# Optimization experiments

Measured on AMD Instinct MI355X. Metric: run time of the kernel, lower is better.

Reference implementation:

```python
import jax, jax.numpy as jnp
import numpy as np

N = 50000
E = 500000
CH = 256
H1, C1 = 4, 64
H2, C2 = 8, 32
CONCAT = H1 * C1 + H2 * C2  # 512


def setup_inputs() -> dict:
    key = jax.random.key(0)
    ks = jax.random.split(key, 16)
    s = 0.05
    x = jax.random.normal(ks[0], (N, CH), dtype=jnp.float32)
    edge_index = jax.random.randint(ks[1], (2, E), 0, N, dtype=jnp.int64)
    return {
        "x": x,
        "edge_index": edge_index,
        "gamma": jnp.ones((CH,), jnp.float32),
        "beta": jnp.zeros((CH,), jnp.float32),
        "W1": jax.random.normal(ks[2], (CH, H1 * C1), jnp.float32) * s,
        "a_src1": jax.random.normal(ks[3], (H1, C1), jnp.float32) * s,
        "a_dst1": jax.random.normal(ks[4], (H1, C1), jnp.float32) * s,
        "b1": jnp.zeros((H1 * C1,), jnp.float32),
        "W2": jax.random.normal(ks[5], (CH, H2 * C2), jnp.float32) * s,
        "a_src2": jax.random.normal(ks[6], (H2, C2), jnp.float32) * s,
        "a_dst2": jax.random.normal(ks[7], (H2, C2), jnp.float32) * s,
        "b2": jnp.zeros((H2 * C2,), jnp.float32),
        "Wu": jax.random.normal(ks[8], (CONCAT, CH), jnp.float32) * s,
        "bu": jnp.zeros((CH,), jnp.float32),
    }


def _layer_norm(x, gamma, beta, eps=1e-5):
    mu = jnp.mean(x, axis=-1, keepdims=True)
    var = jnp.var(x, axis=-1, keepdims=True)
    return (x - mu) * jax.lax.rsqrt(var + eps) * gamma + beta


def _gat_conv(x, src, dst, W, a_src, a_dst, bias, heads, out_ch, n_nodes):
    # x: [N, CH] -> per-head projection h: [N, H, C]
    h = (x @ W).reshape(n_nodes, heads, out_ch)
    alpha_s = jnp.einsum('nhc,hc->nh', h, a_src)  # [N, H]
    alpha_d = jnp.einsum('nhc,hc->nh', h, a_dst)  # [N, H]
    e = jax.nn.leaky_relu(alpha_s[src] + alpha_d[dst], negative_slope=0.2)  # [E, H]
    # segment softmax over incoming edges of each dst node (self-loops guarantee nonempty segments)
    m = jax.ops.segment_max(e, dst, num_segments=n_nodes)
    ex = jnp.exp(e - m[dst])
    denom = jax.ops.segment_sum(ex, dst, num_segments=n_nodes)
    a = ex / (denom[dst] + 1e-16)  # [E, H]
    msg = h[src] * a[:, :, None]  # [E, H, C]
    out = jax.ops.segment_sum(msg, dst, num_segments=n_nodes)  # [N, H, C]
    return out.reshape(n_nodes, heads * out_ch) + bias


def reference(x, edge_index, gamma, beta, W1, a_src1, a_dst1, b1,
              W2, a_src2, a_dst2, b2, Wu, bu):
    n = x.shape[0]
    # add self-loops (PyG GATConv default)
    loop = jnp.arange(n, dtype=edge_index.dtype)
    src = jnp.concatenate([edge_index[0], loop])
    dst = jnp.concatenate([edge_index[1], loop])

    residual = x
    x_norm = _layer_norm(x, gamma, beta)
    out1 = _gat_conv(x_norm, src, dst, W1, a_src1, a_dst1, b1, H1, C1, n)
    out2 = _gat_conv(x_norm, src, dst, W2, a_src2, a_dst2, b2, H2, C2, n)
    x_cat = jax.nn.elu(jnp.concatenate([out1, out2], axis=-1))
    unified = x_cat @ Wu + bu
    return residual + unified
```

## Files before the change

### kernel.cpp

```cpp
#include <hip/hip_runtime.h>
#include <hip/hip_bf16.h>
#include <math.h>

constexpr int CH = 256;
constexpr int CC = 512;
constexpr int AP = 16;
constexpr int HS = 576;

typedef __bf16 bf16x8 __attribute__((ext_vector_type(8)));
typedef float  f32x4  __attribute__((ext_vector_type(4)));
typedef float  f32x2  __attribute__((ext_vector_type(2)));
typedef int    i32x4  __attribute__((ext_vector_type(4)));
typedef __attribute__((address_space(3))) void lds_void;
typedef __attribute__((address_space(1))) void glb_void;

__device__ inline unsigned short f2bf(float f) {
    union { float f; unsigned u; } v; v.f = f;
    unsigned r = v.u + 0x7FFFu + ((v.u >> 16) & 1u);
    return (unsigned short)(r >> 16);
}
__device__ __host__ inline int perm_s2l(int s) {
    return (s & ~31) + 16 * (s & 1) + ((s & 31) >> 1);
}

__global__ void fused_pre_kernel(const float* __restrict__ x, const float* __restrict__ gamma,
                                 const float* __restrict__ beta,
                                 const float* __restrict__ W1, const float* __restrict__ W2,
                                 const float* __restrict__ Wu,
                                 const float* __restrict__ as1, const float* __restrict__ ad1,
                                 const float* __restrict__ as2, const float* __restrict__ ad2,
                                 const float* __restrict__ b1, const float* __restrict__ b2,
                                 unsigned short* __restrict__ xnb,
                                 unsigned short* __restrict__ WT1, unsigned short* __restrict__ WTu,
                                 unsigned short* __restrict__ Pt, float* __restrict__ bperm,
                                 int* __restrict__ deg,
                                 int N, int LNB) {
    int b = blockIdx.x;
    int t = threadIdx.x;
    if (b < LNB) {
        int wid = b * 4 + (t >> 6);
        int lane = t & 63;
        if (wid >= N) return;
        const float4 v = *(const float4*)(x + (size_t)wid * CH + lane * 4);
        float s = v.x + v.y + v.z + v.w;
        float sq = v.x * v.x + v.y * v.y + v.z * v.z + v.w * v.w;
        #pragma unroll
        for (int o = 32; o; o >>= 1) { s += __shfl_xor(s, o); sq += __shfl_xor(sq, o); }
        float mu = s * (1.0f / CH);
        float var = sq * (1.0f / CH) - mu * mu;
        float rs = rsqrtf(var + 1e-5f);
        float4 g = *(const float4*)(gamma + lane * 4);
        float4 bb = *(const float4*)(beta + lane * 4);
        unsigned short o0 = f2bf((v.x - mu) * rs * g.x + bb.x);
        unsigned short o1 = f2bf((v.y - mu) * rs * g.y + bb.y);
        unsigned short o2 = f2bf((v.z - mu) * rs * g.z + bb.z);
        unsigned short o3 = f2bf((v.w - mu) * rs * g.w + bb.w);
        uint2 pk;
        pk.x = (unsigned)o0 | ((unsigned)o1 << 16);
        pk.y = (unsigned)o2 | ((unsigned)o3 << 16);
        *(uint2*)(xnb + (size_t)wid * CH + lane * 4) = pk;
    } else if (b < LNB + 512) {
        int idx = (b - LNB) * 256 + t;
        int n = idx >> 8, k = idx & 255;
        float v = (n < 256) ? W1[(size_t)k * 256 + n] : W2[(size_t)k * 256 + (n - 256)];
        WT1[idx] = f2bf(v);
    } else if (b < LNB + 1024) {
        int idx = (b - LNB - 512) * 256 + t;
        int n = idx >> 9, ks = idx & 511;
        int kl = perm_s2l(ks);
        WTu[idx] = f2bf(Wu[(size_t)kl * 256 + n]);
    } else if (b < LNB + 1056) {
        int n = b - LNB - 1024;
        int k = t;
        float a = 0.f;
        if (n < 4) {
            for (int c = 0; c < 64; ++c) a += W1[(size_t)k * 256 + n * 64 + c] * as1[n * 64 + c];
        } else if (n < 12) {
            for (int c = 0; c < 32; ++c) a += W2[(size_t)k * 256 + (n - 4) * 32 + c] * as2[(n - 4) * 32 + c];
        } else if (n >= 16 && n < 20) {
            for (int c = 0; c < 64; ++c) a += W1[(size_t)k * 256 + (n - 16) * 64 + c] * ad1[(n - 16) * 64 + c];
        } else if (n >= 20 && n < 28) {
            for (int c = 0; c < 32; ++c) a += W2[(size_t)k * 256 + (n - 20) * 32 + c] * ad2[(n - 20) * 32 + c];
        }
        Pt[n * 256 + k] = f2bf(a);
    } else if (b < LNB + 1058) {
        int ks = (b - LNB - 1056) * 256 + t;
        int kl = perm_s2l(ks);
        bperm[ks] = (kl < 256) ? b1[kl] : b2[kl - 256];
    } else {
        int i = (b - LNB - 1058) * 256 + t;
        if (i < N) deg[i] = 0;
    }
}

template<int K>
__device__ inline void gemm_core32(const unsigned short* __restrict__ Ab,
                                   const unsigned short* __restrict__ Bt,
                                   unsigned short* As, unsigned short* Bs,
                                   f32x4 acc[4][4], int m0, int n0, int M) {
    const int t = threadIdx.x;
    const int lane = t & 63;
    const int wave = t >> 6;
    const int wr = wave >> 1, wc = wave & 1;
    const int rowc = lane >> 2;
    const int eslot = lane & 3;
    const int fr = lane & 15;
    const int fkb = (lane >> 4) << 4;

    auto stage = [&](int buf, int k0) {
        #pragma unroll
        for (int c = 0; c < 2; ++c) {
            int chunk = wave * 2 + c;
            int row = chunk * 16 + rowc;
            int se = ((eslot ^ (row & 3)) << 3);
            int gra = m0 + row; if (gra >= M) gra = M - 1;
            __builtin_amdgcn_global_load_lds((const glb_void*)(Ab + (size_t)gra * K + k0 + se),
                                             (lds_void*)&As[buf * 4096 + chunk * 512], 16, 0, 0);
            __builtin_amdgcn_global_load_lds((const glb_void*)(Bt + (size_t)(n0 + row) * K + k0 + se),
                                             (lds_void*)&Bs[buf * 4096 + chunk * 512], 16, 0, 0);
        }
    };
    auto compute = [&](int buf) {
        const int bb = buf * 8192;
        bf16x8 af[4], bfr[4];
        #pragma unroll
        for (int m = 0; m < 4; ++m) {
            int r = wr * 64 + m * 16 + fr;
            int pc = fkb ^ ((r & 3) << 4);
            af[m] = *(const bf16x8*)((const char*)As + bb + r * 64 + pc);
        }
        #pragma unroll
        for (int n = 0; n < 4; ++n) {
            int r = wc * 64 + n * 16 + fr;
            int pc = fkb ^ ((r & 3) << 4);
            bfr[n] = *(const bf16x8*)((const char*)Bs + bb + r * 64 + pc);
        }
        #pragma unroll
        for (int m = 0; m < 4; ++m)
            #pragma unroll
            for (int n = 0; n < 4; ++n)
                acc[m][n] = __builtin_amdgcn_mfma_f32_16x16x32_bf16(af[m], bfr[n], acc[m][n], 0, 0, 0);
    };

    stage(0, 0);
    __syncthreads();
    int cur = 0;
    #pragma unroll
    for (int k0 = 32; k0 < K; k0 += 32) {
        stage(cur ^ 1, k0);
        compute(cur);
        __syncthreads();
        cur ^= 1;
    }
    compute(cur);
}

__global__ __launch_bounds__(256) void gemm1_mfma(
    const unsigned short* __restrict__ Ab, const unsigned short* __restrict__ Bt,
    const unsigned short* __restrict__ Pt,
    unsigned char* __restrict__ Hq,
    float* __restrict__ alpha_dst, int M, int MB, int G1B,
    const int* __restrict__ dstE, int* __restrict__ deg, int E) {
    __shared__ unsigned short As[8192];
    __shared__ unsigned short Bs[8192];
    const int s = blockIdx.x;
    if (s >= G1B + MB) {
        int i = (s - G1B - MB) * 256 + threadIdx.x;
        if (i < E) atomicAdd(&deg[dstE[i]], 1);
        return;
    }
    const int lane = threadIdx.x & 63;
    const int wave = threadIdx.x >> 6;
    const int fr = lane & 15;
    const int fkb = (lane >> 4) << 4;
    const int orow = (lane >> 4) * 4;

    if (s < G1B) {
        const int xcd = s & 7;
        const int jj = s >> 3;
        const int n_blk = jj & 3;
        const int m_blk = (jj >> 2) * 8 + xcd;
        if (m_blk >= MB) return;
        const int m0 = m_blk * 128, n0 = n_blk * 128;
        const int wr = wave >> 1, wc = wave & 1;
        f32x4 acc[4][4] = {};
        gemm_core32<256>(Ab, Bt, As, Bs, acc, m0, n0, M);
        #pragma unroll
        for (int m = 0; m < 4; ++m)
            #pragma unroll
            for (int j = 0; j < 4; ++j) {
                int r = m0 + wr * 64 + m * 16 + orow + j;
                if (r < M) {
                    #pragma unroll
                    for (int p = 0; p < 2; ++p) {
                        int cst = n0 + wc * 64 + p * 32 + fr * 2;
                        unsigned q = (unsigned)__builtin_amdgcn_cvt_pk_fp8_f32(
                            acc[m][2 * p][j], acc[m][2 * p + 1][j], 0, false);
                        *(unsigned short*)(Hq + (size_t)r * HS + cst) = (unsigned short)q;
                    }
                }
            }
        return;
    }
    const int m_blk = s - G1B;
    if (m_blk >= MB) return;
    const int m0 = m_blk * 128;
    {
        int rr_in = lane >> 5;
        int e32 = lane & 31;
        #pragma unroll
        for (int c = 0; c < 4; ++c) {
            int chunk = wave * 4 + c;
            int rr = chunk * 2 + rr_in;
            const unsigned short* g = Pt + rr * 256 + ((e32 ^ (rr & 7)) << 3);
            __builtin_amdgcn_global_load_lds((const glb_void*)g,
                                             (lds_void*)&Bs[chunk * 512], 16, 0, 0);
        }
    }
    const int rowc = lane >> 2, eslot = lane & 3;
    auto stageA = [&](int buf, int k0) {
        #pragma unroll
        for (int c = 0; c < 2; ++c) {
            int chunk = wave * 2 + c;
            int row = chunk * 16 + rowc;
            int gra = m0 + row; if (gra >= M) gra = M - 1;
            const unsigned short* g = Ab + (size_t)gra * 256 + k0 + ((eslot ^ (row & 3)) << 3);
            __builtin_amdgcn_global_load_lds((const glb_void*)g,
                                             (lds_void*)&As[buf * 4096 + chunk * 512], 16, 0, 0);
        }
    };
    f32x4 a2[2][2] = {};
    auto computeA = [&](int buf, int k0) {
        const int bb = buf * 8192;
        bf16x8 af[2], bf_[2];
        #pragma unroll
        for (int m = 0; m < 2; ++m) {
            int r = wave * 32 + m * 16 + fr;
            int pc = fkb ^ ((r & 3) << 4);
            af[m] = *(const bf16x8*)((const char*)As + bb + r * 64 + pc);
        }
        #pragma unroll
        for (int n = 0; n < 2; ++n) {
            int rb = n * 16 + fr;
            int pcb = (k0 * 2 + fkb) ^ ((rb & 7) << 4);
            bf_[n] = *(const bf16x8*)((const char*)Bs + rb * 512 + pcb);
        }
        #pragma unroll
        for (int m = 0; m < 2; ++m)
            #pragma unroll
            for (int n = 0; n < 2; ++n)
                a2[m][n] = __builtin_amdgcn_mfma_f32_16x16x32_bf16(af[m], bf_[n], a2[m][n], 0, 0, 0);
    };
    stageA(0, 0);
    __syncthreads();
    int cur = 0;
    #pragma unroll
    for (int k0 = 32; k0 < 256; k0 += 32) {
        stageA(cur ^ 1, k0);
        computeA(cur, k0 - 32);
        __syncthreads();
        cur ^= 1;
    }
    computeA(cur, 224);
    #pragma unroll
    for (int m = 0; m < 2; ++m)
        #pragma unroll
        for (int j = 0; j < 4; ++j) {
            int r = m0 + wave * 32 + m * 16 + orow + j;
            if (fr < 12 && r < M) {
                *(float*)(Hq + (size_t)r * HS + 512 + fr * 4) = a2[m][0][j];
                alpha_dst[(size_t)r * AP + fr] = a2[m][1][j];
            }
        }
}

__global__ __launch_bounds__(256) void gemm2_mfma(const unsigned short* __restrict__ Ab,
                                                  const unsigned short* __restrict__ Bt,
                                                  const float* __restrict__ bu,
                                                  const float* __restrict__ xres,
                                                  float* __restrict__ C, int M, int MB) {
    __shared__ unsigned short As[8192];
    __shared__ unsigned short Bs[8192];
    const int s = blockIdx.x;
    const int xcd = s & 7;
    const int jj = s >> 3;
    const int n_blk = jj & 1;
    const int m_blk = (jj >> 1) * 8 + xcd;
    if (m_blk >= MB) return;
    const int m0 = m_blk * 128, n0 = n_blk * 128;
    const int lane = threadIdx.x & 63;
    const int wave = threadIdx.x >> 6;
    const int wr = wave >> 1, wc = wave & 1;
    f32x4 acc[4][4] = {};
    gemm_core32<512>(Ab, Bt, As, Bs, acc, m0, n0, M);
    const int fr = lane & 15;
    const int orow = (lane >> 4) * 4;
    #pragma unroll
    for (int m = 0; m < 4; ++m)
        #pragma unroll
        for (int j = 0; j < 4; ++j) {
            int r = m0 + wr * 64 + m * 16 + orow + j;
            if (r < M) {
                #pragma unroll
                for (int n = 0; n < 4; ++n) {
                    int ccol = n0 + wc * 64 + n * 16 + fr;
                    float xr = __builtin_nontemporal_load(&xres[(size_t)r * CH + ccol]);
                    __builtin_nontemporal_store(acc[m][n][j] + bu[ccol] + xr,
                                                &C[(size_t)r * CH + ccol]);
                }
            }
        }
}

__global__ __launch_bounds__(256) void scan1_kernel(const int* __restrict__ deg, int* __restrict__ pre,
                                                    int* __restrict__ bsum, int n) {
    __shared__ int wsum[4];
    int t = threadIdx.x, lane = t & 63, w = t >> 6;
    int base = blockIdx.x * 1024 + t * 4;
    int v0 = base     < n ? deg[base]     + 1 : 0;
    int v1 = base + 1 < n ? deg[base + 1] + 1 : 0;
    int v2 = base + 2 < n ? deg[base + 2] + 1 : 0;
    int v3 = base + 3 < n ? deg[base + 3] + 1 : 0;
    int s = v0 + v1 + v2 + v3;
    int sc = s;
    #pragma unroll
    for (int o = 1; o < 64; o <<= 1) { int xx = __shfl_up(sc, o); if (lane >= o) sc += xx; }
    if (lane == 63) wsum[w] = sc;
    __syncthreads();
    int wo = 0;
    #pragma unroll
    for (int k = 0; k < 4; ++k) if (k < w) wo += wsum[k];
    int p = wo + sc - s;
    if (base     < n) pre[base]     = p; p += v0;
    if (base + 1 < n) pre[base + 1] = p; p += v1;
    if (base + 2 < n) pre[base + 2] = p; p += v2;
    if (base + 3 < n) pre[base + 3] = p;
    if (t == 255) bsum[blockIdx.x] = wo + sc;
}
__global__ void scan3_csr_kernel(const int* __restrict__ pre, const int* __restrict__ bsum,
                                 int* __restrict__ offsets, int* __restrict__ cursor,
                                 int* __restrict__ csr, int n, int total) {
    int i = blockIdx.x * 256 + threadIdx.x;
    if (i < n) {
        int chunk = i >> 10;
        int boff = 0;
        for (int k = 0; k < chunk; ++k) boff += bsum[k];
        int off = pre[i] + boff;
        offsets[i] = off;
        cursor[i] = off + 1;
        csr[off] = i * HS;
    }
    if (i == 0) offsets[n] = total;
}
__global__ void scatter_kernel(const int* __restrict__ src, const int* __restrict__ dst,
                               int* __restrict__ cursor, int* __restrict__ csr, int E) {
    int i = blockIdx.x * blockDim.x + threadIdx.x;
    if (i < E) {
        int pos = atomicAdd(&cursor[dst[i]], 1);
        csr[pos] = src[i] * HS;
    }
}

__global__ void aggregate_kernel(const unsigned char* __restrict__ Hq,
                                 const float* __restrict__ alpha_dst,
                                 const int* __restrict__ offsets,
                                 const int* __restrict__ csr,
                                 const float* __restrict__ bperm,
                                 unsigned short* __restrict__ xcb, int N) {
    int n = __builtin_amdgcn_readfirstlane((int)((blockIdx.x * blockDim.x + threadIdx.x) >> 6));
    int lane = threadIdx.x & 63;
    if (n >= N) return;
    int beg = offsets[n], end = offsets[n + 1];
    int c0 = lane * 8;
    int hid = (lane < 32) ? (lane >> 3) : (4 + ((lane - 32) >> 2));
    int aoff = 512 + hid * 4;
    float adh = alpha_dst[(size_t)n * AP + hid];

    float ssum = 0.f;
    f32x2 A0 = {0.f, 0.f}, A1 = {0.f, 0.f}, A2 = {0.f, 0.f}, A3 = {0.f, 0.f};

    int i = beg;
    for (; i + 4 <= end; i += 4) {
        int off[4];
        #pragma unroll
        for (int u = 0; u < 4; ++u) off[u] = csr[i + u];
        float lw[4];
        #pragma unroll
        for (int u = 0; u < 4; ++u) lw[u] = *(const float*)(Hq + (size_t)off[u] + aoff);
        uint2 hv[4];
        #pragma unroll
        for (int u = 0; u < 4; ++u) hv[u] = *(const uint2*)(Hq + (size_t)off[u] + c0);
        #pragma unroll
        for (int u = 0; u < 4; ++u) {
            float l = lw[u] + adh;
            l = fmaxf(l, 0.2f * l);
            float wv = __expf(l);
            ssum += wv;
            f32x2 wv2; wv2[0] = wv; wv2[1] = wv;
            A0 += __builtin_amdgcn_cvt_pk_f32_fp8(hv[u].x, false) * wv2;
            A1 += __builtin_amdgcn_cvt_pk_f32_fp8(hv[u].x, true)  * wv2;
            A2 += __builtin_amdgcn_cvt_pk_f32_fp8(hv[u].y, false) * wv2;
            A3 += __builtin_amdgcn_cvt_pk_f32_fp8(hv[u].y, true)  * wv2;
        }
    }
    for (; i < end; ++i) {
        int off = csr[i];
        float l = *(const float*)(Hq + (size_t)off + aoff) + adh;
        uint2 hv0 = *(const uint2*)(Hq + (size_t)off + c0);
        l = fmaxf(l, 0.2f * l);
        float wv = __expf(l);
        ssum += wv;
        f32x2 wv2; wv2[0] = wv; wv2[1] = wv;
        A0 += __builtin_amdgcn_cvt_pk_f32_fp8(hv0.x, false) * wv2;
        A1 += __builtin_amdgcn_cvt_pk_f32_fp8(hv0.x, true)  * wv2;
        A2 += __builtin_amdgcn_cvt_pk_f32_fp8(hv0.y, false) * wv2;
        A3 += __builtin_amdgcn_cvt_pk_f32_fp8(hv0.y, true)  * wv2;
    }

    float inv = 1.0f / (ssum + 1e-16f);
    float4 bb0 = *(const float4*)(bperm + c0);
    float4 bb1 = *(const float4*)(bperm + c0 + 4);
    float o[8];
    o[0] = A0[0] * inv + bb0.x; o[1] = A0[1] * inv + bb0.y;
    o[2] = A1[0] * inv + bb0.z; o[3] = A1[1] * inv + bb0.w;
    o[4] = A2[0] * inv + bb1.x; o[5] = A2[1] * inv + bb1.y;
    o[6] = A3[0] * inv + bb1.z; o[7] = A3[1] * inv + bb1.w;
    #pragma unroll
    for (int j = 0; j < 8; ++j) o[j] = o[j] > 0.f ? o[j] : expm1f(o[j]);
    unsigned short u[8];
    #pragma unroll
    for (int j = 0; j < 8; ++j) u[j] = f2bf(o[j]);
    i32x4 pk;
    pk[0] = (int)((unsigned)u[0] | ((unsigned)u[1] << 16));
    pk[1] = (int)((unsigned)u[2] | ((unsigned)u[3] << 16));
    pk[2] = (int)((unsigned)u[4] | ((unsigned)u[5] << 16));
    pk[3] = (int)((unsigned)u[6] | ((unsigned)u[7] << 16));
    __builtin_nontemporal_store(pk, (i32x4*)(xcb + (size_t)n * CC + c0));
}

extern "C" void kernel_launch(void* const* d_in, const int* in_sizes, int n_in,
                              void* d_out, int out_size, void* d_ws, size_t ws_size,
                              hipStream_t stream) {
    const float* x     = (const float*)d_in[0];
    const int*   ei    = (const int*)d_in[1];
    const float* gamma = (const float*)d_in[2];
    const float* beta  = (const float*)d_in[3];
    const float* W1    = (const float*)d_in[4];
    const float* as1   = (const float*)d_in[5];
    const float* ad1   = (const float*)d_in[6];
    const float* b1    = (const float*)d_in[7];
    const float* W2    = (const float*)d_in[8];
    const float* as2   = (const float*)d_in[9];
    const float* ad2   = (const float*)d_in[10];
    const float* b2    = (const float*)d_in[11];
    const float* Wu    = (const float*)d_in[12];
    const float* bu    = (const float*)d_in[13];
    float* out = (float*)d_out;

    const int N = in_sizes[0] / CH;
    const int E = in_sizes[1] / 2;
    const int* src = ei;
    const int* dst = ei + E;

    char* w = (char*)d_ws;
    auto alloc = [&](size_t bytes) { char* p = w; w += (bytes + 255) & ~(size_t)255; return p; };
    unsigned char*  Hq  = (unsigned char*)alloc((size_t)N * HS);
    unsigned short* xnb = (unsigned short*)alloc((size_t)N * CH * 2);
    unsigned short* xcb = (unsigned short*)alloc((size_t)N * CC * 2);
    unsigned short* WT1 = (unsigned short*)alloc(512 * 256 * 2);
    unsigned short* WTu = (unsigned short*)alloc(256 * 512 * 2);
    unsigned short* Pt  = (unsigned short*)alloc(32 * 256 * 2);
    float* bperm = (float*)alloc(512 * 4);
    float* alpha_dst = (float*)alloc((size_t)N * AP * 4);
    int* deg     = (int*)alloc((size_t)N * 4);
    int* pre     = (int*)alloc((size_t)N * 4);
    int* bsum    = (int*)alloc(64 * 4);
    int* offsets = (int*)alloc(((size_t)N + 1) * 4);
    int* cursor  = (int*)alloc((size_t)N * 4);
    int* csr     = (int*)alloc(((size_t)E + N) * 4);

    const int LNB = (N + 3) / 4;
    const int DEGZ = (N + 255) / 256;
    fused_pre_kernel<<<LNB + 1058 + DEGZ, 256, 0, stream>>>(
        x, gamma, beta, W1, W2, Wu, as1, ad1, as2, ad2, b1, b2,
        xnb, WT1, WTu, Pt, bperm, deg, N, LNB);

    const int MB = (N + 127) / 128;
    const int MB8 = ((MB + 7) / 8) * 8;
    const int G1B = MB8 * 4;
    const int HB = (E + 255) / 256;
    gemm1_mfma<<<G1B + MB + HB, 256, 0, stream>>>(xnb, WT1, Pt, Hq, alpha_dst,
                                                  N, MB, G1B, dst, deg, E);

    int nb = (N + 1023) / 1024;
    scan1_kernel<<<nb, 256, 0, stream>>>(deg, pre, bsum, N);
    scan3_csr_kernel<<<(N + 255) / 256, 256, 0, stream>>>(pre, bsum, offsets, cursor, csr, N, E + N);
    scatter_kernel<<<(E + 255) / 256, 256, 0, stream>>>(src, dst, cursor, csr, E);

    aggregate_kernel<<<(N + 3) / 4, 256, 0, stream>>>(Hq, alpha_dst, offsets, csr,
                                                      bperm, xcb, N);

    gemm2_mfma<<<MB8 * 2, 256, 0, stream>>>(xcb, WTu, bu, x, out, N, MB);
}
```

Before: 191.6 us.

## Replace two-pass degree scan with atomic wave-level segment allocation

The two-kernel exclusive scan (per-block scan plus serial block-offset summation) is replaced by a single kernel. Each wave scans its degrees and reserves a contiguous CSR range with one atomicAdd on a global counter, which removes a launch and the serial bsum loop. CSR segments are no longer in node order, so the aggregate kernel now computes the segment end from deg instead of offsets[n+1]. The degree-histogram blocks in gemm1 also process four edges per thread, which cuts their block count.

```diff
diff --git a/kernel.cpp b/kernel.cpp
--- a/kernel.cpp
+++ b/kernel.cpp
@@ -33,7 +33,7 @@
                                  unsigned short* __restrict__ xnb,
                                  unsigned short* __restrict__ WT1, unsigned short* __restrict__ WTu,
                                  unsigned short* __restrict__ Pt, float* __restrict__ bperm,
-                                 int* __restrict__ deg,
+                                 int* __restrict__ deg, int* __restrict__ counter,
                                  int N, int LNB) {
     int b = blockIdx.x;
     int t = threadIdx.x;
@@ -87,6 +87,7 @@
         int ks = (b - LNB - 1056) * 256 + t;
         int kl = perm_s2l(ks);
         bperm[ks] = (kl < 256) ? b1[kl] : b2[kl - 256];
+        if (ks == 0) counter[0] = 0;
     } else {
         int i = (b - LNB - 1058) * 256 + t;
         if (i < N) deg[i] = 0;
@@ -165,8 +166,12 @@
     __shared__ unsigned short Bs[8192];
     const int s = blockIdx.x;
     if (s >= G1B + MB) {
-        int i = (s - G1B - MB) * 256 + threadIdx.x;
-        if (i < E) atomicAdd(&deg[dstE[i]], 1);
+        int base = (s - G1B - MB) * 1024 + threadIdx.x;
+        #pragma unroll
+        for (int u = 0; u < 4; ++u) {
+            int i = base + u * 256;
+            if (i < E) atomicAdd(&deg[dstE[i]], 1);
+        }
         return;
     }
     const int lane = threadIdx.x & 63;
@@ -312,45 +317,27 @@
         }
 }
 
-__global__ __launch_bounds__(256) void scan1_kernel(const int* __restrict__ deg, int* __restrict__ pre,
-                                                    int* __restrict__ bsum, int n) {
-    __shared__ int wsum[4];
-    int t = threadIdx.x, lane = t & 63, w = t >> 6;
-    int base = blockIdx.x * 1024 + t * 4;
-    int v0 = base     < n ? deg[base]     + 1 : 0;
-    int v1 = base + 1 < n ? deg[base + 1] + 1 : 0;
-    int v2 = base + 2 < n ? deg[base + 2] + 1 : 0;
-    int v3 = base + 3 < n ? deg[base + 3] + 1 : 0;
-    int s = v0 + v1 + v2 + v3;
-    int sc = s;
+__global__ __launch_bounds__(256) void alloc_csr_kernel(const int* __restrict__ deg,
+                                                        int* __restrict__ counter,
+                                                        int* __restrict__ offsets,
+                                                        int* __restrict__ cursor,
+                                                        int* __restrict__ csr, int n) {
+    int i = blockIdx.x * 256 + threadIdx.x;
+    int lane = threadIdx.x & 63;
+    int d = (i < n) ? deg[i] + 1 : 0;
+    int sc = d;
     #pragma unroll
     for (int o = 1; o < 64; o <<= 1) { int xx = __shfl_up(sc, o); if (lane >= o) sc += xx; }
-    if (lane == 63) wsum[w] = sc;
-    __syncthreads();
-    int wo = 0;
-    #pragma unroll
-    for (int k = 0; k < 4; ++k) if (k < w) wo += wsum[k];
-    int p = wo + sc - s;
-    if (base     < n) pre[base]     = p; p += v0;
-    if (base + 1 < n) pre[base + 1] = p; p += v1;
-    if (base + 2 < n) pre[base + 2] = p; p += v2;
-    if (base + 3 < n) pre[base + 3] = p;
-    if (t == 255) bsum[blockIdx.x] = wo + sc;
-}
-__global__ void scan3_csr_kernel(const int* __restrict__ pre, const int* __restrict__ bsum,
-                                 int* __restrict__ offsets, int* __restrict__ cursor,
-                                 int* __restrict__ csr, int n, int total) {
-    int i = blockIdx.x * 256 + threadIdx.x;
+    int waveTot = __shfl(sc, 63);
+    int base = 0;
+    if (lane == 63) base = atomicAdd(counter, waveTot);
+    base = __shfl(base, 63);
     if (i < n) {
-        int chunk = i >> 10;
-        int boff = 0;
-        for (int k = 0; k < chunk; ++k) boff += bsum[k];
-        int off = pre[i] + boff;
+        int off = base + sc - d;
         offsets[i] = off;
         cursor[i] = off + 1;
         csr[off] = i * HS;
     }
-    if (i == 0) offsets[n] = total;
 }
 __global__ void scatter_kernel(const int* __restrict__ src, const int* __restrict__ dst,
                                int* __restrict__ cursor, int* __restrict__ csr, int E) {
@@ -364,13 +351,15 @@
 __global__ void aggregate_kernel(const unsigned char* __restrict__ Hq,
                                  const float* __restrict__ alpha_dst,
                                  const int* __restrict__ offsets,
+                                 const int* __restrict__ deg,
                                  const int* __restrict__ csr,
                                  const float* __restrict__ bperm,
                                  unsigned short* __restrict__ xcb, int N) {
     int n = __builtin_amdgcn_readfirstlane((int)((blockIdx.x * blockDim.x + threadIdx.x) >> 6));
     int lane = threadIdx.x & 63;
     if (n >= N) return;
-    int beg = offsets[n], end = offsets[n + 1];
+    int beg = offsets[n];
+    int end = beg + deg[n] + 1;
     int c0 = lane * 8;
     int hid = (lane < 32) ? (lane >> 3) : (4 + ((lane - 32) >> 2));
     int aoff = 512 + hid * 4;
@@ -473,8 +462,7 @@
     float* bperm = (float*)alloc(512 * 4);
     float* alpha_dst = (float*)alloc((size_t)N * AP * 4);
     int* deg     = (int*)alloc((size_t)N * 4);
-    int* pre     = (int*)alloc((size_t)N * 4);
-    int* bsum    = (int*)alloc(64 * 4);
+    int* counter = (int*)alloc(256);
     int* offsets = (int*)alloc(((size_t)N + 1) * 4);
     int* cursor  = (int*)alloc((size_t)N * 4);
     int* csr     = (int*)alloc(((size_t)E + N) * 4);
@@ -483,21 +471,19 @@
     const int DEGZ = (N + 255) / 256;
     fused_pre_kernel<<<LNB + 1058 + DEGZ, 256, 0, stream>>>(
         x, gamma, beta, W1, W2, Wu, as1, ad1, as2, ad2, b1, b2,
-        xnb, WT1, WTu, Pt, bperm, deg, N, LNB);
+        xnb, WT1, WTu, Pt, bperm, deg, counter, N, LNB);
 
     const int MB = (N + 127) / 128;
     const int MB8 = ((MB + 7) / 8) * 8;
     const int G1B = MB8 * 4;
-    const int HB = (E + 255) / 256;
+    const int HB = (E + 1023) / 1024;
     gemm1_mfma<<<G1B + MB + HB, 256, 0, stream>>>(xnb, WT1, Pt, Hq, alpha_dst,
                                                   N, MB, G1B, dst, deg, E);
 
-    int nb = (N + 1023) / 1024;
-    scan1_kernel<<<nb, 256, 0, stream>>>(deg, pre, bsum, N);
-    scan3_csr_kernel<<<(N + 255) / 256, 256, 0, stream>>>(pre, bsum, offsets, cursor, csr, N, E + N);
+    alloc_csr_kernel<<<(N + 255) / 256, 256, 0, stream>>>(deg, counter, offsets, cursor, csr, N);
     scatter_kernel<<<(E + 255) / 256, 256, 0, stream>>>(src, dst, cursor, csr, E);
 
-    aggregate_kernel<<<(N + 3) / 4, 256, 0, stream>>>(Hq, alpha_dst, offsets, csr,
+    aggregate_kernel<<<(N + 3) / 4, 256, 0, stream>>>(Hq, alpha_dst, offsets, deg, csr,
                                                       bperm, xcb, N);
 
     gemm2_mfma<<<MB8 * 2, 256, 0, stream>>>(xcb, WTu, bu, x, out, N, MB);
```

Result: slower. 196.0 us (+2.3%).
